# Kernel optimization log

Measured on AMD Instinct MI355X. Metric: run time of the kernel, lower is better.

The kernel has to match this reference:

```python
import jax, jax.numpy as jnp
import numpy as np

IMG_SIZE = 32
PATCH_SIZE = 4
GRID = IMG_SIZE // PATCH_SIZE  # 8 -> 64 patches
EMBED = 768
PATCH_DIM = 1 * 3 * PATCH_SIZE * PATCH_SIZE  # 48
BATCH = 1024


def setup_inputs() -> dict:
    key = jax.random.key(0)
    k1, k2, k3, k4 = jax.random.split(key, 4)
    x = jax.random.normal(k1, (BATCH, 1, 3, IMG_SIZE, IMG_SIZE), dtype=jnp.float32)
    W = jax.random.normal(k2, (EMBED, PATCH_DIM), dtype=jnp.float32) * 0.02  # fc1.weight [out,in]
    cls_token = jax.random.normal(k3, (1, EMBED), dtype=jnp.float32)
    pos_emb = jax.random.normal(k4, (1, GRID * GRID + 1, EMBED), dtype=jnp.float32)
    return {"x": x, "W": W, "cls_token": cls_token, "pos_emb": pos_emb}


def reference(x, W, cls_token, pos_emb):
    B, D1, C, H, Wd = x.shape
    # Row-major patch extraction matching the loop (col fast, row slow).
    # patch flatten order = (D1, C, ph, pw), identical to nn.Flatten(1) on [B,D1,C,P,P].
    patches = x.reshape(B, D1, C, GRID, PATCH_SIZE, GRID, PATCH_SIZE)
    patches = patches.transpose(0, 3, 5, 1, 2, 4, 6)  # [B, gr, gc, D1, C, P, P]
    patches = patches.reshape(B, GRID * GRID, D1 * C * PATCH_SIZE * PATCH_SIZE)  # [B,64,48]
    proj = jnp.einsum('bnp,ep->bne', patches, W)  # fc1 (no bias) -> [B,64,E]
    cls = jnp.broadcast_to(cls_token[None, :, :], (B, 1, EMBED))
    s = jnp.concatenate([cls, proj], axis=1)  # [B,65,E]
    return pos_emb + s
```

## Files before the change

### kernel.cpp

```cpp
#include <hip/hip_runtime.h>


#define BATCH   1024
#define EMBED   768
#define NPATCH  64
#define SEQ     65
#define OUTB    (SEQ * EMBED)

typedef __attribute__((ext_vector_type(8))) short bf16x8;
typedef __attribute__((ext_vector_type(4))) float f32x4;

__device__ __forceinline__ short f2bf(float f) {
    union { float f; unsigned u; } v; v.f = f;
    unsigned r = v.u + 0x7FFFu + ((v.u >> 16) & 1u);
    return (short)(r >> 16);
}

__global__ __launch_bounds__(256) void cls_row_kernel(const float* __restrict__ cls,
                                                      const float* __restrict__ pos,
                                                      float* __restrict__ out) {
    int g = blockIdx.x * 256 + threadIdx.x;
    int b = g / 192;
    int j = g - b * 192;
    const float4* c4 = (const float4*)cls;
    const float4* p4 = (const float4*)pos;
    float4 cv = c4[j];
    float4 pv = p4[j];
    float4 o;
    o.x = cv.x + pv.x; o.y = cv.y + pv.y; o.z = cv.z + pv.z; o.w = cv.w + pv.w;
    ((float4*)out)[(size_t)b * (OUTB / 4) + j] = o;
}

__global__ __launch_bounds__(256, 2) void patch_embed_mfma(const float* __restrict__ x,
                                                           const float* __restrict__ W,
                                                           const float* __restrict__ pos,
                                                           float* __restrict__ out) {
    __shared__ short A[64 * 64];

    const int tid  = threadIdx.x;
    const int lane = tid & 63;
    const int wave = tid >> 6;
    const int lr   = lane & 15;
    const int lg   = lane >> 4;
    const int ebase = wave * 192;

    bf16x8 bw[12][2];
    #pragma unroll
    for (int nt = 0; nt < 12; ++nt) {
        const float* wrow = W + (ebase + nt * 16 + lr) * 48;
        #pragma unroll
        for (int kk = 0; kk < 2; ++kk) {
            const int k0 = kk * 32 + lg * 8;
            bf16x8 f = {0, 0, 0, 0, 0, 0, 0, 0};
            if (k0 < 48) {
                float4 u0 = *(const float4*)(wrow + k0);
                float4 u1 = *(const float4*)(wrow + k0 + 4);
                f[0] = f2bf(u0.x); f[1] = f2bf(u0.y); f[2] = f2bf(u0.z); f[3] = f2bf(u0.w);
                f[4] = f2bf(u1.x); f[5] = f2bf(u1.y); f[6] = f2bf(u1.z); f[7] = f2bf(u1.w);
            }
            bw[nt][kk] = f;
        }
    }

    const int b0 = blockIdx.x * 2;

    #pragma unroll 1
    for (int bi = 0; bi < 2; ++bi) {
        const int b = b0 + bi;

        __syncthreads();

        #pragma unroll
        for (int i = 0; i < 2; ++i) {
            const int cid = tid + i * 256;
            const int row = cid >> 3;
            const int kb  = cid & 7;
            short* dst = &A[row * 64 + ((kb ^ (row & 7)) * 8)];
            bf16x8 v = {0, 0, 0, 0, 0, 0, 0, 0};
            if (kb < 6) {
                const int c   = kb >> 1;
                const int ph0 = (kb & 1) * 2;
                const int gr = row >> 3, gc = row & 7;
                const float* src = x + (size_t)b * 3072 + c * 1024 + (gr * 4 + ph0) * 32 + gc * 4;
                float4 u0 = *(const float4*)src;
                float4 u1 = *(const float4*)(src + 32);
                v[0] = f2bf(u0.x); v[1] = f2bf(u0.y); v[2] = f2bf(u0.z); v[3] = f2bf(u0.w);
                v[4] = f2bf(u1.x); v[5] = f2bf(u1.y); v[6] = f2bf(u1.z); v[7] = f2bf(u1.w);
            }
            *(bf16x8*)dst = v;
        }
        __syncthreads();

        const size_t outbase = (size_t)b * OUTB + EMBED;
        #pragma unroll 1
        for (int mt = 0; mt < 4; ++mt) {
            const int arow = mt * 16 + lr;
            const int sw0  = ((0 * 4 + lg) ^ (arow & 7)) * 8;
            const int sw1  = ((1 * 4 + lg) ^ (arow & 7)) * 8;
            bf16x8 a0 = *(const bf16x8*)&A[arow * 64 + sw0];
            bf16x8 a1 = *(const bf16x8*)&A[arow * 64 + sw1];

            f32x4 acc[12];
            const f32x4 zero = {0.f, 0.f, 0.f, 0.f};
            #pragma unroll
            for (int nt = 0; nt < 12; ++nt)
                acc[nt] = __builtin_amdgcn_mfma_f32_16x16x32_bf16(a0, bw[nt][0], zero, 0, 0, 0);
            #pragma unroll
            for (int nt = 0; nt < 12; ++nt)
                acc[nt] = __builtin_amdgcn_mfma_f32_16x16x32_bf16(a1, bw[nt][1], acc[nt], 0, 0, 0);

            #pragma unroll
            for (int j = 0; j < 4; ++j) {
                const int n = mt * 16 + lg * 4 + j;
                const float* prow = pos + (size_t)(n + 1) * EMBED + ebase + lr;
                float* orow = out + outbase + (size_t)n * EMBED + ebase + lr;
                #pragma unroll
                for (int nt = 0; nt < 12; ++nt)
                    orow[nt * 16] = acc[nt][j] + prow[nt * 16];
            }
        }
    }
}

extern "C" void kernel_launch(void* const* d_in, const int* in_sizes, int n_in,
                              void* d_out, int out_size, void* d_ws, size_t ws_size,
                              hipStream_t stream) {
    const float* x   = (const float*)d_in[0];
    const float* W   = (const float*)d_in[1];
    const float* cls = (const float*)d_in[2];
    const float* pos = (const float*)d_in[3];
    float* out = (float*)d_out;

    hipLaunchKernelGGL(cls_row_kernel, dim3(BATCH * (EMBED / 4) / 256), dim3(256), 0, stream,
                       cls, pos, out);
    hipLaunchKernelGGL(patch_embed_mfma, dim3(BATCH / 2), dim3(256), 0, stream,
                       x, W, pos, out);
}
```

Before: 48.78 us.

## Fuse cls row into patch-embed kernel, one batch per 512-thread block

Merges the separate cls-token kernel into the MFMA patch-embedding kernel, which removes one launch. Each block now handles a single image with 8 waves, and each wave covers 96 embedding columns instead of 192. The A-tile staging overlaps with the per-block W register loads, and output stores use nontemporal hints. In exchange, every block reloads and converts its W slice, and twice as many blocks repeat that work.

New measurement: 60.26 us. 1.24x slower.

```diff
diff --git a/kernel.cpp b/kernel.cpp
--- a/kernel.cpp
+++ b/kernel.cpp
@@ -16,25 +16,11 @@
     return (short)(r >> 16);
 }
 
-__global__ __launch_bounds__(256) void cls_row_kernel(const float* __restrict__ cls,
-                                                      const float* __restrict__ pos,
-                                                      float* __restrict__ out) {
-    int g = blockIdx.x * 256 + threadIdx.x;
-    int b = g / 192;
-    int j = g - b * 192;
-    const float4* c4 = (const float4*)cls;
-    const float4* p4 = (const float4*)pos;
-    float4 cv = c4[j];
-    float4 pv = p4[j];
-    float4 o;
-    o.x = cv.x + pv.x; o.y = cv.y + pv.y; o.z = cv.z + pv.z; o.w = cv.w + pv.w;
-    ((float4*)out)[(size_t)b * (OUTB / 4) + j] = o;
-}
-
-__global__ __launch_bounds__(256, 2) void patch_embed_mfma(const float* __restrict__ x,
-                                                           const float* __restrict__ W,
-                                                           const float* __restrict__ pos,
-                                                           float* __restrict__ out) {
+__global__ __launch_bounds__(512, 4) void patch_embed_fused(const float* __restrict__ x,
+                                                            const float* __restrict__ W,
+                                                            const float* __restrict__ cls,
+                                                            const float* __restrict__ pos,
+                                                            float* __restrict__ out) {
     __shared__ short A[64 * 64];
 
     const int tid  = threadIdx.x;
@@ -42,11 +28,37 @@
     const int wave = tid >> 6;
     const int lr   = lane & 15;
     const int lg   = lane >> 4;
-    const int ebase = wave * 192;
+    const int ebase = wave * 96;
+    const int b = blockIdx.x;
 
-    bf16x8 bw[12][2];
+    if (tid < 192) {
+        f32x4 cv = ((const f32x4*)cls)[tid];
+        f32x4 pv = ((const f32x4*)pos)[tid];
+        f32x4 o = cv + pv;
+        __builtin_nontemporal_store(o, (f32x4*)out + (size_t)b * (OUTB / 4) + tid);
+    }
+
+    {
+        const int row = tid >> 3;
+        const int kb  = tid & 7;
+        short* dst = &A[row * 64 + ((kb ^ (row & 7)) * 8)];
+        bf16x8 v = {0, 0, 0, 0, 0, 0, 0, 0};
+        if (kb < 6) {
+            const int c   = kb >> 1;
+            const int ph0 = (kb & 1) * 2;
+            const int gr = row >> 3, gc = row & 7;
+            const float* src = x + (size_t)b * 3072 + c * 1024 + (gr * 4 + ph0) * 32 + gc * 4;
+            float4 u0 = *(const float4*)src;
+            float4 u1 = *(const float4*)(src + 32);
+            v[0] = f2bf(u0.x); v[1] = f2bf(u0.y); v[2] = f2bf(u0.z); v[3] = f2bf(u0.w);
+            v[4] = f2bf(u1.x); v[5] = f2bf(u1.y); v[6] = f2bf(u1.z); v[7] = f2bf(u1.w);
+        }
+        *(bf16x8*)dst = v;
+    }
+
+    bf16x8 bw[6][2];
     #pragma unroll
-    for (int nt = 0; nt < 12; ++nt) {
+    for (int nt = 0; nt < 6; ++nt) {
         const float* wrow = W + (ebase + nt * 16 + lr) * 48;
         #pragma unroll
         for (int kk = 0; kk < 2; ++kk) {
@@ -62,62 +74,34 @@
         }
     }
 
-    const int b0 = blockIdx.x * 2;
+    __syncthreads();
 
+    const size_t outbase = (size_t)b * OUTB + EMBED;
     #pragma unroll 1
-    for (int bi = 0; bi < 2; ++bi) {
-        const int b = b0 + bi;
+    for (int mt = 0; mt < 4; ++mt) {
+        const int arow = mt * 16 + lr;
+        const int sw0  = ((0 * 4 + lg) ^ (arow & 7)) * 8;
+        const int sw1  = ((1 * 4 + lg) ^ (arow & 7)) * 8;
+        bf16x8 a0 = *(const bf16x8*)&A[arow * 64 + sw0];
+        bf16x8 a1 = *(const bf16x8*)&A[arow * 64 + sw1];
 
-        __syncthreads();
+        f32x4 acc[6];
+        const f32x4 zero = {0.f, 0.f, 0.f, 0.f};
+        #pragma unroll
+        for (int nt = 0; nt < 6; ++nt)
+            acc[nt] = __builtin_amdgcn_mfma_f32_16x16x32_bf16(a0, bw[nt][0], zero, 0, 0, 0);
+        #pragma unroll
+        for (int nt = 0; nt < 6; ++nt)
+            acc[nt] = __builtin_amdgcn_mfma_f32_16x16x32_bf16(a1, bw[nt][1], acc[nt], 0, 0, 0);
 
         #pragma unroll
-        for (int i = 0; i < 2; ++i) {
-            const int cid = tid + i * 256;
-            const int row = cid >> 3;
-            const int kb  = cid & 7;
-            short* dst = &A[row * 64 + ((kb ^ (row & 7)) * 8)];
-            bf16x8 v = {0, 0, 0, 0, 0, 0, 0, 0};
-            if (kb < 6) {
-                const int c   = kb >> 1;
-                const int ph0 = (kb & 1) * 2;
-                const int gr = row >> 3, gc = row & 7;
-                const float* src = x + (size_t)b * 3072 + c * 1024 + (gr * 4 + ph0) * 32 + gc * 4;
-                float4 u0 = *(const float4*)src;
-                float4 u1 = *(const float4*)(src + 32);
-                v[0] = f2bf(u0.x); v[1] = f2bf(u0.y); v[2] = f2bf(u0.z); v[3] = f2bf(u0.w);
-                v[4] = f2bf(u1.x); v[5] = f2bf(u1.y); v[6] = f2bf(u1.z); v[7] = f2bf(u1.w);
-            }
-            *(bf16x8*)dst = v;
-        }
-        __syncthreads();
-
-        const size_t outbase = (size_t)b * OUTB + EMBED;
-        #pragma unroll 1
-        for (int mt = 0; mt < 4; ++mt) {
-            const int arow = mt * 16 + lr;
-            const int sw0  = ((0 * 4 + lg) ^ (arow & 7)) * 8;
-            const int sw1  = ((1 * 4 + lg) ^ (arow & 7)) * 8;
-            bf16x8 a0 = *(const bf16x8*)&A[arow * 64 + sw0];
-            bf16x8 a1 = *(const bf16x8*)&A[arow * 64 + sw1];
-
-            f32x4 acc[12];
-            const f32x4 zero = {0.f, 0.f, 0.f, 0.f};
+        for (int j = 0; j < 4; ++j) {
+            const int n = mt * 16 + lg * 4 + j;
+            const float* prow = pos + (size_t)(n + 1) * EMBED + ebase + lr;
+            float* orow = out + outbase + (size_t)n * EMBED + ebase + lr;
             #pragma unroll
-            for (int nt = 0; nt < 12; ++nt)
-                acc[nt] = __builtin_amdgcn_mfma_f32_16x16x32_bf16(a0, bw[nt][0], zero, 0, 0, 0);
-            #pragma unroll
-            for (int nt = 0; nt < 12; ++nt)
-                acc[nt] = __builtin_amdgcn_mfma_f32_16x16x32_bf16(a1, bw[nt][1], acc[nt], 0, 0, 0);
-
-            #pragma unroll
-            for (int j = 0; j < 4; ++j) {
-                const int n = mt * 16 + lg * 4 + j;
-                const float* prow = pos + (size_t)(n + 1) * EMBED + ebase + lr;
-                float* orow = out + outbase + (size_t)n * EMBED + ebase + lr;
-                #pragma unroll
-                for (int nt = 0; nt < 12; ++nt)
-                    orow[nt * 16] = acc[nt][j] + prow[nt * 16];
-            }
+            for (int nt = 0; nt < 6; ++nt)
+                __builtin_nontemporal_store(acc[nt][j] + prow[nt * 16], orow + nt * 16);
         }
     }
 }
@@ -131,8 +115,6 @@
     const float* pos = (const float*)d_in[3];
     float* out = (float*)d_out;
 
-    hipLaunchKernelGGL(cls_row_kernel, dim3(BATCH * (EMBED / 4) / 256), dim3(256), 0, stream,
-                       cls, pos, out);
-    hipLaunchKernelGGL(patch_embed_mfma, dim3(BATCH / 2), dim3(256), 0, stream,
-                       x, W, pos, out);
+    hipLaunchKernelGGL(patch_embed_fused, dim3(BATCH), dim3(512), 0, stream,
+                       x, W, cls, pos, out);
 }
```
